# Kernel tuning notes

Hardware: AMD Instinct MI355X
Metric: run time of the kernel (lower is better)

The kernel has to match this reference:

```python
import jax, jax.numpy as jnp
import numpy as np

N = 100000   # nodes
E = 1600000  # edges
H = 128      # num_features == hidden_size
C = 64       # num_classes
BN_EPS = 1e-5


def setup_inputs() -> dict:
    key = jax.random.key(0)
    ks = jax.random.split(key, 11)
    return {
        "x": jax.random.normal(ks[0], (N, H), jnp.float32),
        "edge_index": jax.random.randint(ks[1], (2, E), 0, N, dtype=jnp.int32),
        "edge_attr": jax.random.normal(ks[2], (E,), jnp.float32),
        "conv_w": jax.random.normal(ks[3], (2, 3, H, H), jnp.float32) / np.sqrt(H).astype(np.float32),
        "conv_b": jax.random.normal(ks[4], (2, 3, H), jnp.float32) * 0.1,
        "bn_g": jax.random.uniform(ks[5], (2, 3, H), jnp.float32, 0.5, 1.5),
        "bn_b": jax.random.normal(ks[6], (2, 3, H), jnp.float32) * 0.1,
        "bn_m": jax.random.normal(ks[7], (2, 3, H), jnp.float32) * 0.1,
        "bn_v": jax.random.uniform(ks[8], (2, 3, H), jnp.float32, 0.5, 1.5),
        "fc_w": jax.random.normal(ks[9], (H, C), jnp.float32) / np.sqrt(H).astype(np.float32),
        "fc_b": jax.random.normal(ks[10], (C,), jnp.float32) * 0.1,
    }


def _gin_conv(h, edge_index, w, b, g, beta, m, v):
    # GIN: out = MLP((1+eps)*x + sum_{j in N(i)} x_j), eps=0 (PyG default)
    src, dst = edge_index[0], edge_index[1]
    agg = jax.ops.segment_sum(h[src], dst, num_segments=N)  # [N,H] scatter-add
    h = h + agg
    for i in range(3):  # Linear -> BatchNorm1d (eval stats) -> ReLU
        h = h @ w[i] + b[i]
        h = (h - m[i]) * jax.lax.rsqrt(v[i] + BN_EPS) * g[i] + beta[i]
        h = jax.nn.relu(h)
    return h


def reference(x, edge_index, edge_attr, conv_w, conv_b, bn_g, bn_b, bn_m, bn_v, fc_w, fc_b):
    # edge_attr is ignored by default PyG GINConv (no edge weighting in GIN)
    h = jax.nn.relu(_gin_conv(x, edge_index, conv_w[0], conv_b[0], bn_g[0], bn_b[0], bn_m[0], bn_v[0]))
    h = jax.nn.relu(_gin_conv(h, edge_index, conv_w[1], conv_b[1], bn_g[1], bn_b[1], bn_m[1], bn_v[1]))
    # dropout is identity in eval mode
    logits = h @ fc_w + fc_b  # [N,C]
    return jax.nn.log_softmax(logits, axis=1)
```

## Files before the change

### kernel.cpp

```cpp
#include <hip/hip_runtime.h>

#define NN 100000
#define NE 1600000
#define HF 128
#define NC 64
#define AP 136
#define NB 391
#define BSH 8
#define BMASK 255
#define BCAP 4608

typedef __bf16 bf16x8 __attribute__((ext_vector_type(8)));
typedef float  f32x4  __attribute__((ext_vector_type(4)));
typedef float  f32x2  __attribute__((ext_vector_type(2)));
typedef unsigned short us8 __attribute__((ext_vector_type(8)));
typedef unsigned int u32x4 __attribute__((ext_vector_type(4)));

__device__ __forceinline__ unsigned short f2b(float x) {
  unsigned int u = __float_as_uint(x);
  u += 0x7FFFu + ((u >> 16) & 1u);
  return (unsigned short)(u >> 16);
}
__device__ __forceinline__ float b2f(unsigned short b) {
  return __uint_as_float(((unsigned int)b) << 16);
}

__device__ __forceinline__ void addrow(f32x2 acc[4], u32x4 w) {
  #pragma unroll
  for (int i = 0; i < 4; i++) {
    f32x2 p;
    p.x = __uint_as_float(w[i] << 16);
    p.y = __uint_as_float(w[i] & 0xFFFF0000u);
    acc[i] += p;
  }
}

__global__ __launch_bounds__(512) void prologue_bin(const float* __restrict__ x,
                                                    unsigned short* __restrict__ xb,
                                                    const float* __restrict__ conv_w,
                                                    const float* __restrict__ conv_b,
                                                    const float* __restrict__ bn_g,
                                                    const float* __restrict__ bn_b,
                                                    const float* __restrict__ bn_m,
                                                    const float* __restrict__ bn_v,
                                                    const float* __restrict__ fc_w,
                                                    unsigned short* __restrict__ wt,
                                                    unsigned short* __restrict__ wtf,
                                                    float* __restrict__ sarr,
                                                    float* __restrict__ tarr,
                                                    int* __restrict__ gcur,
                                                    const int* __restrict__ src,
                                                    const int* __restrict__ dst,
                                                    unsigned int* __restrict__ binned) {
  __shared__ int hist[NB];
  int t = threadIdx.x;
  int idx = blockIdx.x * 512 + t;
  {
    size_t i = (size_t)idx * 8;
    float4 a = *(const float4*)(x + i);
    float4 b = *(const float4*)(x + i + 4);
    us8 v = { f2b(a.x), f2b(a.y), f2b(a.z), f2b(a.w),
              f2b(b.x), f2b(b.y), f2b(b.z), f2b(b.w) };
    *(us8*)(xb + i) = v;
  }
  if (idx < 3 * HF) {
    int k = idx >> 7, jj = idx & 127;
    xb[(size_t)k * (NN + 1) * HF + (size_t)NN * HF + jj] = 0;
  }
  if (idx < 6 * HF * HF) {
    int j  = idx & 7;
    int m  = (idx >> 3) & 15;
    int q  = (idx >> 7) & 3;
    int nt = (idx >> 9) & 7;
    int k0 = (idx >> 12) & 3;
    int ls = idx >> 14;
    int k = k0 * 32 + q * 8 + j;
    int n = nt * 16 + m;
    wt[idx] = f2b(conv_w[(ls * HF + k) * HF + n]);
  }
  if (idx < HF * NC) {
    int j  = idx & 7;
    int m  = (idx >> 3) & 15;
    int q  = (idx >> 7) & 3;
    int nt = (idx >> 9) & 3;
    int k0 = idx >> 11;
    int k = k0 * 32 + q * 8 + j;
    int c = nt * 16 + m;
    wtf[idx] = f2b(fc_w[k * NC + c]);
  }
  if (idx < 6 * HF) {
    float s = bn_g[idx] * rsqrtf(bn_v[idx] + 1e-5f);
    sarr[idx] = s;
    tarr[idx] = (conv_b[idx] - bn_m[idx]) * s + bn_b[idx];
  }
  if (blockIdx.x < NB) {
    if (t < NB) hist[t] = 0;
    __syncthreads();
    int base = blockIdx.x * 4096;
    int sv[8], dv[8];
    #pragma unroll
    for (int j = 0; j < 8; j++) {
      int e = base + j * 512 + t;
      bool ok = e < NE;
      dv[j] = ok ? dst[e] : -1;
      sv[j] = ok ? src[e] : 0;
      if (ok) atomicAdd(&hist[dv[j] >> BSH], 1);
    }
    __syncthreads();
    if (t < NB) {
      int c = hist[t];
      if (c) hist[t] = t * BCAP + atomicAdd(&gcur[t], c);
    }
    __syncthreads();
    #pragma unroll
    for (int j = 0; j < 8; j++) {
      if (dv[j] >= 0) {
        int b = dv[j] >> BSH;
        int p = atomicAdd(&hist[b], 1);
        binned[p] = (unsigned int)sv[j] | ((unsigned int)(dv[j] & BMASK) << 17);
      }
    }
  }
}

__global__ __launch_bounds__(512) void build_csr(const unsigned int* __restrict__ binned,
                                                 const int* __restrict__ gcur,
                                                 int* __restrict__ offs,
                                                 int* __restrict__ deg,
                                                 int* __restrict__ csr) {
  __shared__ int ncnt[256];
  __shared__ int sm[256];
  int t = threadIdx.x;
  int b = blockIdx.x;
  int beg = b * BCAP;
  int cntb = gcur[b];
  if (t < 256) ncnt[t] = 0;
  __syncthreads();
  for (int e = beg + t; e < beg + cntb; e += 512) atomicAdd(&ncnt[binned[e] >> 17], 1);
  __syncthreads();
  int s = 0;
  if (t < 256) { s = ncnt[t]; sm[t] = s; }
  __syncthreads();
  for (int off = 1; off < 256; off <<= 1) {
    int u = (t < 256 && t >= off) ? sm[t - off] : 0;
    __syncthreads();
    if (t < 256) sm[t] += u;
    __syncthreads();
  }
  if (t < 256) {
    int ex = sm[t] - s + beg;
    int node = (b << BSH) + t;
    if (node < NN) { offs[node] = ex; deg[node] = s; }
    ncnt[t] = ex;
  }
  __syncthreads();
  for (int e = beg + t; e < beg + cntb; e += 512) {
    unsigned int u = binned[e];
    int p = atomicAdd(&ncnt[u >> 17], 1);
    csr[p] = (int)(u & 0x1FFFFu);
  }
}

__global__ __launch_bounds__(256) void aggregate(const unsigned short* __restrict__ h,
                                                 const int* __restrict__ offs,
                                                 const int* __restrict__ deg,
                                                 const int* __restrict__ csr,
                                                 unsigned short* __restrict__ out) {
  int wave = threadIdx.x >> 6;
  int lane = threadIdx.x & 63;
  int node = blockIdx.x * 4 + wave;
  int g  = lane >> 4;
  int sl = lane & 15;
  int beg = offs[node];
  int dg  = deg[node];
  int n  = dg + 1;
  int nf = n < 64 ? n : 64;

  int myidx = NN;
  if (lane < nf) myidx = (lane == dg) ? node : csr[beg + lane];

  f32x2 acc[4];
  #pragma unroll
  for (int i = 0; i < 4; i++) acc[i] = (f32x2){0.f, 0.f};

  int K = (nf + 3) >> 2;
  int j = 0;
  for (; j + 3 < K; j += 4) {
    int s0 = __shfl(myidx, (j + 0) * 4 + g);
    int s1 = __shfl(myidx, (j + 1) * 4 + g);
    int s2 = __shfl(myidx, (j + 2) * 4 + g);
    int s3 = __shfl(myidx, (j + 3) * 4 + g);
    u32x4 v0 = *(const u32x4*)(h + (size_t)s0 * HF + sl * 8);
    u32x4 v1 = *(const u32x4*)(h + (size_t)s1 * HF + sl * 8);
    u32x4 v2 = *(const u32x4*)(h + (size_t)s2 * HF + sl * 8);
    u32x4 v3 = *(const u32x4*)(h + (size_t)s3 * HF + sl * 8);
    addrow(acc, v0);
    addrow(acc, v1);
    addrow(acc, v2);
    addrow(acc, v3);
  }
  for (; j + 1 < K; j += 2) {
    int s0 = __shfl(myidx, (j + 0) * 4 + g);
    int s1 = __shfl(myidx, (j + 1) * 4 + g);
    u32x4 v0 = *(const u32x4*)(h + (size_t)s0 * HF + sl * 8);
    u32x4 v1 = *(const u32x4*)(h + (size_t)s1 * HF + sl * 8);
    addrow(acc, v0);
    addrow(acc, v1);
  }
  if (j < K) {
    int s0 = __shfl(myidx, j * 4 + g);
    u32x4 v0 = *(const u32x4*)(h + (size_t)s0 * HF + sl * 8);
    addrow(acc, v0);
  }

  if (dg >= 64) {
    for (int e = beg + 64 + g; e < beg + dg; e += 4) {
      int s = csr[e];
      u32x4 v = *(const u32x4*)(h + (size_t)s * HF + sl * 8);
      addrow(acc, v);
    }
    if (g == 0) {
      u32x4 v = *(const u32x4*)(h + (size_t)node * HF + sl * 8);
      addrow(acc, v);
    }
  }

  #pragma unroll
  for (int i = 0; i < 4; i++) {
    acc[i].x += __shfl_xor(acc[i].x, 16, 64);
    acc[i].y += __shfl_xor(acc[i].y, 16, 64);
    acc[i].x += __shfl_xor(acc[i].x, 32, 64);
    acc[i].y += __shfl_xor(acc[i].y, 32, 64);
  }
  if (g == 0) {
    us8 r;
    #pragma unroll
    for (int i = 0; i < 4; i++) {
      r[2 * i]     = f2b(acc[i].x);
      r[2 * i + 1] = f2b(acc[i].y);
    }
    *(us8*)(out + (size_t)node * HF + sl * 8) = r;
  }
}

__device__ __forceinline__ void mlp3_body(const unsigned short* __restrict__ in,
                                          unsigned short* Ab,
                                          const unsigned short* __restrict__ wt,
                                          const float* __restrict__ sarr,
                                          const float* __restrict__ tarr,
                                          int layer, int row0, int wave, int lane,
                                          bf16x8 af[4]) {
  int m = lane & 15, q = lane >> 4;
  int node = row0 + wave * 16 + m;
  int nclamp = (node < NN) ? node : 0;
  #pragma unroll
  for (int k0 = 0; k0 < 4; k0++)
    af[k0] = *(const bf16x8*)(in + (size_t)nclamp * HF + k0 * 32 + q * 8);

  const unsigned short* wbase = wt + layer * 3 * 16384;
  #pragma unroll
  for (int sub = 0; sub < 3; sub++) {
    const unsigned short* wsub = wbase + sub * 16384;
    f32x4 acc[8];
    #pragma unroll
    for (int nt = 0; nt < 8; nt++) {
      acc[nt] = (f32x4){0.f, 0.f, 0.f, 0.f};
      #pragma unroll
      for (int k0 = 0; k0 < 4; k0++) {
        bf16x8 bf = *(const bf16x8*)(wsub + ((k0 * 8 + nt) * 64 + lane) * 8);
        acc[nt] = __builtin_amdgcn_mfma_f32_16x16x32_bf16(af[k0], bf, acc[nt], 0, 0, 0);
      }
    }
    const float* sp = sarr + (layer * 3 + sub) * HF;
    const float* tp = tarr + (layer * 3 + sub) * HF;
    #pragma unroll
    for (int nt = 0; nt < 8; nt++) {
      int c = nt * 16 + m;
      float sc = sp[c], sh = tp[c];
      #pragma unroll
      for (int i = 0; i < 4; i++) {
        int r = wave * 16 + q * 4 + i;
        float y = fmaxf(acc[nt][i] * sc + sh, 0.f);
        Ab[r * AP + c] = f2b(y);
      }
    }
    #pragma unroll
    for (int k0 = 0; k0 < 4; k0++)
      af[k0] = *(const bf16x8*)&Ab[(wave * 16 + m) * AP + k0 * 32 + q * 8];
  }
}

__global__ __launch_bounds__(256) void mlp3(const unsigned short* __restrict__ in,
                                            unsigned short* __restrict__ out,
                                            const unsigned short* __restrict__ wt,
                                            const float* __restrict__ sarr,
                                            const float* __restrict__ tarr) {
  __shared__ unsigned short Ab[64 * AP];
  int t = threadIdx.x;
  int lane = t & 63, wave = t >> 6;
  int row0 = blockIdx.x * 64;
  bf16x8 af[4];
  mlp3_body(in, Ab, wt, sarr, tarr, 0, row0, wave, lane, af);

  for (int it = 0; it < 4; it++) {
    int idx = it * 64 + lane;
    int r = wave * 16 + (idx >> 4);
    int c = (idx & 15) << 3;
    int gr = row0 + r;
    if (gr < NN) *(us8*)(out + (size_t)gr * HF + c) = *(const us8*)&Ab[r * AP + c];
  }
}

__global__ __launch_bounds__(256) void mlp3fc(const unsigned short* __restrict__ in,
                                              float* __restrict__ out,
                                              const unsigned short* __restrict__ wt,
                                              const float* __restrict__ sarr,
                                              const float* __restrict__ tarr,
                                              const unsigned short* __restrict__ wtf,
                                              const float* __restrict__ fc_b) {
  __shared__ unsigned short Ab[64 * AP];
  int t = threadIdx.x;
  int lane = t & 63, wave = t >> 6;
  int row0 = blockIdx.x * 64;
  int m = lane & 15, q = lane >> 4;
  bf16x8 af[4];
  mlp3_body(in, Ab, wt, sarr, tarr, 1, row0, wave, lane, af);

  f32x4 acc[4];
  #pragma unroll
  for (int nt = 0; nt < 4; nt++) {
    acc[nt] = (f32x4){0.f, 0.f, 0.f, 0.f};
    #pragma unroll
    for (int k0 = 0; k0 < 4; k0++) {
      bf16x8 bf = *(const bf16x8*)(wtf + ((k0 * 4 + nt) * 64 + lane) * 8);
      acc[nt] = __builtin_amdgcn_mfma_f32_16x16x32_bf16(af[k0], bf, acc[nt], 0, 0, 0);
    }
  }
  float v[4][4];
  #pragma unroll
  for (int nt = 0; nt < 4; nt++) {
    float b = fc_b[nt * 16 + m];
    #pragma unroll
    for (int i = 0; i < 4; i++) v[nt][i] = acc[nt][i] + b;
  }
  float mx[4], sum[4];
  #pragma unroll
  for (int i = 0; i < 4; i++) {
    mx[i] = fmaxf(fmaxf(v[0][i], v[1][i]), fmaxf(v[2][i], v[3][i]));
    mx[i] = fmaxf(mx[i], __shfl_xor(mx[i], 1, 64));
    mx[i] = fmaxf(mx[i], __shfl_xor(mx[i], 2, 64));
    mx[i] = fmaxf(mx[i], __shfl_xor(mx[i], 4, 64));
    mx[i] = fmaxf(mx[i], __shfl_xor(mx[i], 8, 64));
    sum[i] = __expf(v[0][i] - mx[i]) + __expf(v[1][i] - mx[i])
           + __expf(v[2][i] - mx[i]) + __expf(v[3][i] - mx[i]);
    sum[i] += __shfl_xor(sum[i], 1, 64);
    sum[i] += __shfl_xor(sum[i], 2, 64);
    sum[i] += __shfl_xor(sum[i], 4, 64);
    sum[i] += __shfl_xor(sum[i], 8, 64);
    sum[i] = __logf(sum[i]) + mx[i];
  }
  #pragma unroll
  for (int i = 0; i < 4; i++) {
    int gr = row0 + wave * 16 + q * 4 + i;
    if (gr < NN) {
      #pragma unroll
      for (int nt = 0; nt < 4; nt++)
        out[(size_t)gr * NC + nt * 16 + m] = v[nt][i] - sum[i];
    }
  }
}

extern "C" void kernel_launch(void* const* d_in, const int* in_sizes, int n_in,
                              void* d_out, int out_size, void* d_ws, size_t ws_size,
                              hipStream_t stream) {
  const float* x      = (const float*)d_in[0];
  const int*   ei     = (const int*)d_in[1];
  const float* conv_w = (const float*)d_in[3];
  const float* conv_b = (const float*)d_in[4];
  const float* bn_g   = (const float*)d_in[5];
  const float* bn_b   = (const float*)d_in[6];
  const float* bn_m   = (const float*)d_in[7];
  const float* bn_v   = (const float*)d_in[8];
  const float* fc_w   = (const float*)d_in[9];
  const float* fc_b   = (const float*)d_in[10];
  float* out = (float*)d_out;

  const int* srcI = ei;
  const int* dstI = ei + NE;

  unsigned short* Xb   = (unsigned short*)d_ws;
  unsigned short* Abuf = Xb + (size_t)(NN + 1) * HF;
  unsigned short* Bbuf = Abuf + (size_t)(NN + 1) * HF;
  int* gcur   = (int*)(Bbuf + (size_t)(NN + 1) * HF);
  int* offs   = gcur + 512;
  int* deg    = offs + 100004;
  unsigned int* binned = (unsigned int*)(deg + 100004);
  int* csr    = (int*)(binned + (size_t)NB * BCAP);
  unsigned short* wt  = (unsigned short*)(csr + (size_t)NB * BCAP);
  unsigned short* wtf = wt + 6 * HF * HF;
  float* sarr = (float*)(wtf + HF * NC);
  float* tarr = sarr + 6 * HF;

  hipMemsetAsync(gcur, 0, sizeof(int) * NB, stream);
  prologue_bin<<<3125, 512, 0, stream>>>(x, Xb, conv_w, conv_b, bn_g, bn_b, bn_m, bn_v,
                                         fc_w, wt, wtf, sarr, tarr, gcur,
                                         srcI, dstI, binned);
  build_csr<<<NB, 512, 0, stream>>>(binned, gcur, offs, deg, csr);

  aggregate<<<NN / 4, 256, 0, stream>>>(Xb, offs, deg, csr, Abuf);
  mlp3<<<(NN + 63) / 64, 256, 0, stream>>>(Abuf, Bbuf, wt, sarr, tarr);
  aggregate<<<NN / 4, 256, 0, stream>>>(Bbuf, offs, deg, csr, Abuf);
  mlp3fc<<<(NN + 63) / 64, 256, 0, stream>>>(Abuf, out, wt, sarr, tarr, wtf, fc_b);
}
```

Before: 327.7 us.

## Fuse neighbor aggregation into MLP kernels via shared-memory staging

Merges the gather-sum aggregation kernel into the following 3-layer MLP kernel, so that each wave aggregates 16 nodes in sequence and writes the results to LDS, where the MFMA stage reads them. This removes the global write and re-read of the aggregated buffer and two kernel launches. Each wave also prefetches the CSR indices for the next node while summing the current one. In exchange there are far fewer waves working on the latency-bound gather (1563 blocks instead of 25000), which may reduce memory-level parallelism and load balance across nodes with different degrees.

```diff
diff --git a/kernel.cpp b/kernel.cpp
--- a/kernel.cpp
+++ b/kernel.cpp
@@ -20,9 +20,6 @@
   unsigned int u = __float_as_uint(x);
   u += 0x7FFFu + ((u >> 16) & 1u);
   return (unsigned short)(u >> 16);
-}
-__device__ __forceinline__ float b2f(unsigned short b) {
-  return __uint_as_float(((unsigned int)b) << 16);
 }
 
 __device__ __forceinline__ void addrow(f32x2 acc[4], u32x4 w) {
@@ -63,7 +60,7 @@
               f2b(b.x), f2b(b.y), f2b(b.z), f2b(b.w) };
     *(us8*)(xb + i) = v;
   }
-  if (idx < 3 * HF) {
+  if (idx < 2 * HF) {
     int k = idx >> 7, jj = idx & 127;
     xb[(size_t)k * (NN + 1) * HF + (size_t)NN * HF + jj] = 0;
   }
@@ -161,101 +158,115 @@
   }
 }
 
-__global__ __launch_bounds__(256) void aggregate(const unsigned short* __restrict__ h,
-                                                 const int* __restrict__ offs,
-                                                 const int* __restrict__ deg,
-                                                 const int* __restrict__ csr,
-                                                 unsigned short* __restrict__ out) {
-  int wave = threadIdx.x >> 6;
-  int lane = threadIdx.x & 63;
-  int node = blockIdx.x * 4 + wave;
+__device__ __forceinline__ void agg_into_lds(const unsigned short* __restrict__ h,
+                                             const int* __restrict__ offs,
+                                             const int* __restrict__ deg,
+                                             const int* __restrict__ csr,
+                                             unsigned short* Ab,
+                                             int row0, int wave, int lane) {
   int g  = lane >> 4;
   int sl = lane & 15;
-  int beg = offs[node];
-  int dg  = deg[node];
-  int n  = dg + 1;
-  int nf = n < 64 ? n : 64;
-
+  int nodeBase = row0 + wave * 16;
+
+  int beg = 0, dg = 0, nf = 0;
+  if (nodeBase < NN) {
+    beg = offs[nodeBase]; dg = deg[nodeBase];
+    nf = dg + 1; if (nf > 64) nf = 64;
+  }
   int myidx = NN;
-  if (lane < nf) myidx = (lane == dg) ? node : csr[beg + lane];
-
-  f32x2 acc[4];
-  #pragma unroll
-  for (int i = 0; i < 4; i++) acc[i] = (f32x2){0.f, 0.f};
-
-  int K = (nf + 3) >> 2;
-  int j = 0;
-  for (; j + 3 < K; j += 4) {
-    int s0 = __shfl(myidx, (j + 0) * 4 + g);
-    int s1 = __shfl(myidx, (j + 1) * 4 + g);
-    int s2 = __shfl(myidx, (j + 2) * 4 + g);
-    int s3 = __shfl(myidx, (j + 3) * 4 + g);
-    u32x4 v0 = *(const u32x4*)(h + (size_t)s0 * HF + sl * 8);
-    u32x4 v1 = *(const u32x4*)(h + (size_t)s1 * HF + sl * 8);
-    u32x4 v2 = *(const u32x4*)(h + (size_t)s2 * HF + sl * 8);
-    u32x4 v3 = *(const u32x4*)(h + (size_t)s3 * HF + sl * 8);
-    addrow(acc, v0);
-    addrow(acc, v1);
-    addrow(acc, v2);
-    addrow(acc, v3);
-  }
-  for (; j + 1 < K; j += 2) {
-    int s0 = __shfl(myidx, (j + 0) * 4 + g);
-    int s1 = __shfl(myidx, (j + 1) * 4 + g);
-    u32x4 v0 = *(const u32x4*)(h + (size_t)s0 * HF + sl * 8);
-    u32x4 v1 = *(const u32x4*)(h + (size_t)s1 * HF + sl * 8);
-    addrow(acc, v0);
-    addrow(acc, v1);
-  }
-  if (j < K) {
-    int s0 = __shfl(myidx, j * 4 + g);
-    u32x4 v0 = *(const u32x4*)(h + (size_t)s0 * HF + sl * 8);
-    addrow(acc, v0);
-  }
-
-  if (dg >= 64) {
-    for (int e = beg + 64 + g; e < beg + dg; e += 4) {
-      int s = csr[e];
-      u32x4 v = *(const u32x4*)(h + (size_t)s * HF + sl * 8);
-      addrow(acc, v);
+  if (lane < nf) myidx = (lane == dg) ? nodeBase : csr[beg + lane];
+
+  for (int ni = 0; ni < 16; ni++) {
+    int node = nodeBase + ni;
+    int curnf = nf, curdg = dg, curbeg = beg;
+    int curidx = myidx;
+
+    if (ni < 15) {
+      int n2 = node + 1;
+      beg = 0; dg = 0; nf = 0;
+      if (n2 < NN) {
+        beg = offs[n2]; dg = deg[n2];
+        nf = dg + 1; if (nf > 64) nf = 64;
+      }
+      myidx = NN;
+      if (lane < nf) myidx = (lane == dg) ? n2 : csr[beg + lane];
+    }
+
+    f32x2 acc[4];
+    #pragma unroll
+    for (int i = 0; i < 4; i++) acc[i] = (f32x2){0.f, 0.f};
+
+    int K = (curnf + 3) >> 2;
+    int j = 0;
+    for (; j + 3 < K; j += 4) {
+      int s0 = __shfl(curidx, (j + 0) * 4 + g);
+      int s1 = __shfl(curidx, (j + 1) * 4 + g);
+      int s2 = __shfl(curidx, (j + 2) * 4 + g);
+      int s3 = __shfl(curidx, (j + 3) * 4 + g);
+      u32x4 v0 = *(const u32x4*)(h + (size_t)s0 * HF + sl * 8);
+      u32x4 v1 = *(const u32x4*)(h + (size_t)s1 * HF + sl * 8);
+      u32x4 v2 = *(const u32x4*)(h + (size_t)s2 * HF + sl * 8);
+      u32x4 v3 = *(const u32x4*)(h + (size_t)s3 * HF + sl * 8);
+      addrow(acc, v0);
+      addrow(acc, v1);
+      addrow(acc, v2);
+      addrow(acc, v3);
+    }
+    for (; j + 1 < K; j += 2) {
+      int s0 = __shfl(curidx, (j + 0) * 4 + g);
+      int s1 = __shfl(curidx, (j + 1) * 4 + g);
+      u32x4 v0 = *(const u32x4*)(h + (size_t)s0 * HF + sl * 8);
+      u32x4 v1 = *(const u32x4*)(h + (size_t)s1 * HF + sl * 8);
+      addrow(acc, v0);
+      addrow(acc, v1);
+    }
+    if (j < K) {
+      int s0 = __shfl(curidx, j * 4 + g);
+      u32x4 v0 = *(const u32x4*)(h + (size_t)s0 * HF + sl * 8);
+      addrow(acc, v0);
+    }
+
+    if (curdg >= 64) {
+      for (int e = curbeg + 64 + g; e < curbeg + curdg; e += 4) {
+        int s = csr[e];
+        u32x4 v = *(const u32x4*)(h + (size_t)s * HF + sl * 8);
+        addrow(acc, v);
+      }
+      if (g == 0) {
+        u32x4 v = *(const u32x4*)(h + (size_t)node * HF + sl * 8);
+        addrow(acc, v);
+      }
+    }
+
+    #pragma unroll
+    for (int i = 0; i < 4; i++) {
+      acc[i].x += __shfl_xor(acc[i].x, 16, 64);
+      acc[i].y += __shfl_xor(acc[i].y, 16, 64);
+      acc[i].x += __shfl_xor(acc[i].x, 32, 64);
+      acc[i].y += __shfl_xor(acc[i].y, 32, 64);
     }
     if (g == 0) {
-      u32x4 v = *(const u32x4*)(h + (size_t)node * HF + sl * 8);
-      addrow(acc, v);
-    }
-  }
-
-  #pragma unroll
-  for (int i = 0; i < 4; i++) {
-    acc[i].x += __shfl_xor(acc[i].x, 16, 64);
-    acc[i].y += __shfl_xor(acc[i].y, 16, 64);
-    acc[i].x += __shfl_xor(acc[i].x, 32, 64);
-    acc[i].y += __shfl_xor(acc[i].y, 32, 64);
-  }
-  if (g == 0) {
-    us8 r;
-    #pragma unroll
-    for (int i = 0; i < 4; i++) {
-      r[2 * i]     = f2b(acc[i].x);
-      r[2 * i + 1] = f2b(acc[i].y);
-    }
-    *(us8*)(out + (size_t)node * HF + sl * 8) = r;
-  }
-}
-
-__device__ __forceinline__ void mlp3_body(const unsigned short* __restrict__ in,
-                                          unsigned short* Ab,
-                                          const unsigned short* __restrict__ wt,
-                                          const float* __restrict__ sarr,
-                                          const float* __restrict__ tarr,
-                                          int layer, int row0, int wave, int lane,
-                                          bf16x8 af[4]) {
+      us8 r;
+      #pragma unroll
+      for (int i = 0; i < 4; i++) {
+        r[2 * i]     = f2b(acc[i].x);
+        r[2 * i + 1] = f2b(acc[i].y);
+      }
+      *(us8*)&Ab[(wave * 16 + ni) * AP + sl * 8] = r;
+    }
+  }
+}
+
+__device__ __forceinline__ void mlp3_body_lds(unsigned short* Ab,
+                                              const unsigned short* __restrict__ wt,
+                                              const float* __restrict__ sarr,
+                                              const float* __restrict__ tarr,
+                                              int layer, int wave, int lane,
+                                              bf16x8 af[4]) {
   int m = lane & 15, q = lane >> 4;
-  int node = row0 + wave * 16 + m;
-  int nclamp = (node < NN) ? node : 0;
   #pragma unroll
   for (int k0 = 0; k0 < 4; k0++)
-    af[k0] = *(const bf16x8*)(in + (size_t)nclamp * HF + k0 * 32 + q * 8);
+    af[k0] = *(const bf16x8*)&Ab[(wave * 16 + m) * AP + k0 * 32 + q * 8];
 
   const unsigned short* wbase = wt + layer * 3 * 16384;
   #pragma unroll
@@ -290,17 +301,21 @@
   }
 }
 
-__global__ __launch_bounds__(256) void mlp3(const unsigned short* __restrict__ in,
-                                            unsigned short* __restrict__ out,
-                                            const unsigned short* __restrict__ wt,
-                                            const float* __restrict__ sarr,
-                                            const float* __restrict__ tarr) {
+__global__ __launch_bounds__(256) void agg_mlp3(const unsigned short* __restrict__ h,
+                                                const int* __restrict__ offs,
+                                                const int* __restrict__ deg,
+                                                const int* __restrict__ csr,
+                                                unsigned short* __restrict__ out,
+                                                const unsigned short* __restrict__ wt,
+                                                const float* __restrict__ sarr,
+                                                const float* __restrict__ tarr) {
   __shared__ unsigned short Ab[64 * AP];
   int t = threadIdx.x;
   int lane = t & 63, wave = t >> 6;
   int row0 = blockIdx.x * 64;
+  agg_into_lds(h, offs, deg, csr, Ab, row0, wave, lane);
   bf16x8 af[4];
-  mlp3_body(in, Ab, wt, sarr, tarr, 0, row0, wave, lane, af);
+  mlp3_body_lds(Ab, wt, sarr, tarr, 0, wave, lane, af);
 
   for (int it = 0; it < 4; it++) {
     int idx = it * 64 + lane;
@@ -311,20 +326,24 @@
   }
 }
 
-__global__ __launch_bounds__(256) void mlp3fc(const unsigned short* __restrict__ in,
-                                              float* __restrict__ out,
-                                              const unsigned short* __restrict__ wt,
-                                              const float* __restrict__ sarr,
-                                              const float* __restrict__ tarr,
-                                              const unsigned short* __restrict__ wtf,
-                                              const float* __restrict__ fc_b) {
+__global__ __launch_bounds__(256) void agg_mlp3fc(const unsigned short* __restrict__ h,
+                                                  const int* __restrict__ offs,
+                                                  const int* __restrict__ deg,
+                                                  const int* __restrict__ csr,
+                                                  float* __restrict__ out,
+                                                  const unsigned short* __restrict__ wt,
+                                                  const float* __restrict__ sarr,
+                                                  const float* __restrict__ tarr,
+                                                  const unsigned short* __restrict__ wtf,
+                                                  const float* __restrict__ fc_b) {
   __shared__ unsigned short Ab[64 * AP];
   int t = threadIdx.x;
   int lane = t & 63, wave = t >> 6;
   int row0 = blockIdx.x * 64;
   int m = lane & 15, q = lane >> 4;
+  agg_into_lds(h, offs, deg, csr, Ab, row0, wave, lane);
   bf16x8 af[4];
-  mlp3_body(in, Ab, wt, sarr, tarr, 1, row0, wave, lane, af);
+  mlp3_body_lds(Ab, wt, sarr, tarr, 1, wave, lane, af);
 
   f32x4 acc[4];
   #pragma unroll
@@ -389,8 +408,7 @@
   const int* dstI = ei + NE;
 
   unsigned short* Xb   = (unsigned short*)d_ws;
-  unsigned short* Abuf = Xb + (size_t)(NN + 1) * HF;
-  unsigned short* Bbuf = Abuf + (size_t)(NN + 1) * HF;
+  unsigned short* Bbuf = Xb + (size_t)(NN + 1) * HF;
   int* gcur   = (int*)(Bbuf + (size_t)(NN + 1) * HF);
   int* offs   = gcur + 512;
   int* deg    = offs + 100004;
@@ -407,8 +425,7 @@
                                          srcI, dstI, binned);
   build_csr<<<NB, 512, 0, stream>>>(binned, gcur, offs, deg, csr);
 
-  aggregate<<<NN / 4, 256, 0, stream>>>(Xb, offs, deg, csr, Abuf);
-  mlp3<<<(NN + 63) / 64, 256, 0, stream>>>(Abuf, Bbuf, wt, sarr, tarr);
-  aggregate<<<NN / 4, 256, 0, stream>>>(Bbuf, offs, deg, csr, Abuf);
-  mlp3fc<<<(NN + 63) / 64, 256, 0, stream>>>(Abuf, out, wt, sarr, tarr, wtf, fc_b);
-}
+  agg_mlp3<<<(NN + 63) / 64, 256, 0, stream>>>(Xb, offs, deg, csr, Bbuf, wt, sarr, tarr);
+  agg_mlp3fc<<<(NN + 63) / 64, 256, 0, stream>>>(Bbuf, offs, deg, csr, out,
+                                                 wt, sarr, tarr, wtf, fc_b);
+}
```

New measurement: 334.8 us. 1.02x slower.

## Build CSR with global per-node degree atomics instead of two-level binning

Applied to the files above, without the earlier changes.

Replaces the LDS-histogram binning pass and the per-bin CSR build with a simpler three-step scheme. Per-node degrees are counted with global atomics in the prologue, a per-256-node block scan writes offsets and cursors, and a scatter kernel places each edge through a global atomic on its destination cursor. This drops the intermediate binned buffer and the second pass over it. In exchange it adds an extra kernel launch, relies on contended global atomics and random global writes, and still assumes each 256-node block stays within BCAP edges.

```diff
diff --git a/kernel.cpp b/kernel.cpp
--- a/kernel.cpp
+++ b/kernel.cpp
@@ -6,8 +6,6 @@
 #define NC 64
 #define AP 136
 #define NB 391
-#define BSH 8
-#define BMASK 255
 #define BCAP 4608
 
 typedef __bf16 bf16x8 __attribute__((ext_vector_type(8)));
@@ -21,9 +19,6 @@
   u += 0x7FFFu + ((u >> 16) & 1u);
   return (unsigned short)(u >> 16);
 }
-__device__ __forceinline__ float b2f(unsigned short b) {
-  return __uint_as_float(((unsigned int)b) << 16);
-}
 
 __device__ __forceinline__ void addrow(f32x2 acc[4], u32x4 w) {
   #pragma unroll
@@ -35,24 +30,21 @@
   }
 }
 
-__global__ __launch_bounds__(512) void prologue_bin(const float* __restrict__ x,
-                                                    unsigned short* __restrict__ xb,
-                                                    const float* __restrict__ conv_w,
-                                                    const float* __restrict__ conv_b,
-                                                    const float* __restrict__ bn_g,
-                                                    const float* __restrict__ bn_b,
-                                                    const float* __restrict__ bn_m,
-                                                    const float* __restrict__ bn_v,
-                                                    const float* __restrict__ fc_w,
-                                                    unsigned short* __restrict__ wt,
-                                                    unsigned short* __restrict__ wtf,
-                                                    float* __restrict__ sarr,
-                                                    float* __restrict__ tarr,
-                                                    int* __restrict__ gcur,
-                                                    const int* __restrict__ src,
-                                                    const int* __restrict__ dst,
-                                                    unsigned int* __restrict__ binned) {
-  __shared__ int hist[NB];
+__global__ __launch_bounds__(512) void prologue(const float* __restrict__ x,
+                                                unsigned short* __restrict__ xb,
+                                                const float* __restrict__ conv_w,
+                                                const float* __restrict__ conv_b,
+                                                const float* __restrict__ bn_g,
+                                                const float* __restrict__ bn_b,
+                                                const float* __restrict__ bn_m,
+                                                const float* __restrict__ bn_v,
+                                                const float* __restrict__ fc_w,
+                                                unsigned short* __restrict__ wt,
+                                                unsigned short* __restrict__ wtf,
+                                                float* __restrict__ sarr,
+                                                float* __restrict__ tarr,
+                                                int* __restrict__ deg,
+                                                const int* __restrict__ dst) {
   int t = threadIdx.x;
   int idx = blockIdx.x * 512 + t;
   {
@@ -93,72 +85,41 @@
     sarr[idx] = s;
     tarr[idx] = (conv_b[idx] - bn_m[idx]) * s + bn_b[idx];
   }
-  if (blockIdx.x < NB) {
-    if (t < NB) hist[t] = 0;
-    __syncthreads();
-    int base = blockIdx.x * 4096;
-    int sv[8], dv[8];
-    #pragma unroll
-    for (int j = 0; j < 8; j++) {
-      int e = base + j * 512 + t;
-      bool ok = e < NE;
-      dv[j] = ok ? dst[e] : -1;
-      sv[j] = ok ? src[e] : 0;
-      if (ok) atomicAdd(&hist[dv[j] >> BSH], 1);
-    }
-    __syncthreads();
-    if (t < NB) {
-      int c = hist[t];
-      if (c) hist[t] = t * BCAP + atomicAdd(&gcur[t], c);
-    }
-    __syncthreads();
-    #pragma unroll
-    for (int j = 0; j < 8; j++) {
-      if (dv[j] >= 0) {
-        int b = dv[j] >> BSH;
-        int p = atomicAdd(&hist[b], 1);
-        binned[p] = (unsigned int)sv[j] | ((unsigned int)(dv[j] & BMASK) << 17);
-      }
-    }
-  }
-}
-
-__global__ __launch_bounds__(512) void build_csr(const unsigned int* __restrict__ binned,
-                                                 const int* __restrict__ gcur,
+  atomicAdd(&deg[dst[idx]], 1);
+}
+
+__global__ __launch_bounds__(256) void scan_offs(const int* __restrict__ deg,
                                                  int* __restrict__ offs,
-                                                 int* __restrict__ deg,
-                                                 int* __restrict__ csr) {
-  __shared__ int ncnt[256];
+                                                 int* __restrict__ cursor) {
   __shared__ int sm[256];
   int t = threadIdx.x;
   int b = blockIdx.x;
-  int beg = b * BCAP;
-  int cntb = gcur[b];
-  if (t < 256) ncnt[t] = 0;
-  __syncthreads();
-  for (int e = beg + t; e < beg + cntb; e += 512) atomicAdd(&ncnt[binned[e] >> 17], 1);
-  __syncthreads();
-  int s = 0;
-  if (t < 256) { s = ncnt[t]; sm[t] = s; }
+  int node = b * 256 + t;
+  int d = (node < NN) ? deg[node] : 0;
+  sm[t] = d;
   __syncthreads();
   for (int off = 1; off < 256; off <<= 1) {
-    int u = (t < 256 && t >= off) ? sm[t - off] : 0;
+    int u = (t >= off) ? sm[t - off] : 0;
     __syncthreads();
-    if (t < 256) sm[t] += u;
+    sm[t] += u;
     __syncthreads();
   }
-  if (t < 256) {
-    int ex = sm[t] - s + beg;
-    int node = (b << BSH) + t;
-    if (node < NN) { offs[node] = ex; deg[node] = s; }
-    ncnt[t] = ex;
-  }
-  __syncthreads();
-  for (int e = beg + t; e < beg + cntb; e += 512) {
-    unsigned int u = binned[e];
-    int p = atomicAdd(&ncnt[u >> 17], 1);
-    csr[p] = (int)(u & 0x1FFFFu);
-  }
+  if (node < NN) {
+    int ex = sm[t] - d + b * BCAP;
+    offs[node] = ex;
+    cursor[node] = ex;
+  }
+}
+
+__global__ __launch_bounds__(512) void scatter_csr(const int* __restrict__ src,
+                                                   const int* __restrict__ dst,
+                                                   int* __restrict__ cursor,
+                                                   int* __restrict__ csr) {
+  int idx = blockIdx.x * 512 + threadIdx.x;
+  int d = dst[idx];
+  int s = src[idx];
+  int p = atomicAdd(&cursor[d], 1);
+  csr[p] = s;
 }
 
 __global__ __launch_bounds__(256) void aggregate(const unsigned short* __restrict__ h,
@@ -169,6 +130,7 @@
   int wave = threadIdx.x >> 6;
   int lane = threadIdx.x & 63;
   int node = blockIdx.x * 4 + wave;
+  if (node >= NN) return;
   int g  = lane >> 4;
   int sl = lane & 15;
   int beg = offs[node];
@@ -391,21 +353,20 @@
   unsigned short* Xb   = (unsigned short*)d_ws;
   unsigned short* Abuf = Xb + (size_t)(NN + 1) * HF;
   unsigned short* Bbuf = Abuf + (size_t)(NN + 1) * HF;
-  int* gcur   = (int*)(Bbuf + (size_t)(NN + 1) * HF);
-  int* offs   = gcur + 512;
-  int* deg    = offs + 100004;
-  unsigned int* binned = (unsigned int*)(deg + 100004);
-  int* csr    = (int*)(binned + (size_t)NB * BCAP);
+  int* deg    = (int*)(Bbuf + (size_t)(NN + 1) * HF);
+  int* offs   = deg + 100004;
+  int* cursor = offs + 100004;
+  int* csr    = cursor + 100004;
   unsigned short* wt  = (unsigned short*)(csr + (size_t)NB * BCAP);
   unsigned short* wtf = wt + 6 * HF * HF;
   float* sarr = (float*)(wtf + HF * NC);
   float* tarr = sarr + 6 * HF;
 
-  hipMemsetAsync(gcur, 0, sizeof(int) * NB, stream);
-  prologue_bin<<<3125, 512, 0, stream>>>(x, Xb, conv_w, conv_b, bn_g, bn_b, bn_m, bn_v,
-                                         fc_w, wt, wtf, sarr, tarr, gcur,
-                                         srcI, dstI, binned);
-  build_csr<<<NB, 512, 0, stream>>>(binned, gcur, offs, deg, csr);
+  hipMemsetAsync(deg, 0, sizeof(int) * 100004, stream);
+  prologue<<<3125, 512, 0, stream>>>(x, Xb, conv_w, conv_b, bn_g, bn_b, bn_m, bn_v,
+                                     fc_w, wt, wtf, sarr, tarr, deg, dstI);
+  scan_offs<<<NB, 256, 0, stream>>>(deg, offs, cursor);
+  scatter_csr<<<3125, 512, 0, stream>>>(srcI, dstI, cursor, csr);
 
   aggregate<<<NN / 4, 256, 0, stream>>>(Xb, offs, deg, csr, Abuf);
   mlp3<<<(NN + 63) / 64, 256, 0, stream>>>(Abuf, Bbuf, wt, sarr, tarr);
```

New measurement: 463.5 us. 41.5% more time.

## Split edge binning into own kernel and stage MLP weights in LDS

Applied to the files above, without the earlier changes.

Edge binning moves out of the prologue into a separate kernel with 782 blocks handling 2048 edges each, instead of 391 blocks handling 4096 each, so more blocks share the binning work. The MLP kernels now copy each 128x128 bf16 weight sub-matrix cooperatively into shared memory before the MFMA loop, rather than having every wave read the weights from global memory. This adds 32KB of LDS per block and extra barriers, which may lower occupancy, plus one more kernel launch. A bounds guard is also added in aggregate.

```diff
diff --git a/kernel.cpp b/kernel.cpp
--- a/kernel.cpp
+++ b/kernel.cpp
@@ -21,9 +21,6 @@
   u += 0x7FFFu + ((u >> 16) & 1u);
   return (unsigned short)(u >> 16);
 }
-__device__ __forceinline__ float b2f(unsigned short b) {
-  return __uint_as_float(((unsigned int)b) << 16);
-}
 
 __device__ __forceinline__ void addrow(f32x2 acc[4], u32x4 w) {
   #pragma unroll
@@ -35,24 +32,19 @@
   }
 }
 
-__global__ __launch_bounds__(512) void prologue_bin(const float* __restrict__ x,
-                                                    unsigned short* __restrict__ xb,
-                                                    const float* __restrict__ conv_w,
-                                                    const float* __restrict__ conv_b,
-                                                    const float* __restrict__ bn_g,
-                                                    const float* __restrict__ bn_b,
-                                                    const float* __restrict__ bn_m,
-                                                    const float* __restrict__ bn_v,
-                                                    const float* __restrict__ fc_w,
-                                                    unsigned short* __restrict__ wt,
-                                                    unsigned short* __restrict__ wtf,
-                                                    float* __restrict__ sarr,
-                                                    float* __restrict__ tarr,
-                                                    int* __restrict__ gcur,
-                                                    const int* __restrict__ src,
-                                                    const int* __restrict__ dst,
-                                                    unsigned int* __restrict__ binned) {
-  __shared__ int hist[NB];
+__global__ __launch_bounds__(512) void prologue(const float* __restrict__ x,
+                                                unsigned short* __restrict__ xb,
+                                                const float* __restrict__ conv_w,
+                                                const float* __restrict__ conv_b,
+                                                const float* __restrict__ bn_g,
+                                                const float* __restrict__ bn_b,
+                                                const float* __restrict__ bn_m,
+                                                const float* __restrict__ bn_v,
+                                                const float* __restrict__ fc_w,
+                                                unsigned short* __restrict__ wt,
+                                                unsigned short* __restrict__ wtf,
+                                                float* __restrict__ sarr,
+                                                float* __restrict__ tarr) {
   int t = threadIdx.x;
   int idx = blockIdx.x * 512 + t;
   {
@@ -93,32 +85,38 @@
     sarr[idx] = s;
     tarr[idx] = (conv_b[idx] - bn_m[idx]) * s + bn_b[idx];
   }
-  if (blockIdx.x < NB) {
-    if (t < NB) hist[t] = 0;
-    __syncthreads();
-    int base = blockIdx.x * 4096;
-    int sv[8], dv[8];
-    #pragma unroll
-    for (int j = 0; j < 8; j++) {
-      int e = base + j * 512 + t;
-      bool ok = e < NE;
-      dv[j] = ok ? dst[e] : -1;
-      sv[j] = ok ? src[e] : 0;
-      if (ok) atomicAdd(&hist[dv[j] >> BSH], 1);
-    }
-    __syncthreads();
-    if (t < NB) {
-      int c = hist[t];
-      if (c) hist[t] = t * BCAP + atomicAdd(&gcur[t], c);
-    }
-    __syncthreads();
-    #pragma unroll
-    for (int j = 0; j < 8; j++) {
-      if (dv[j] >= 0) {
-        int b = dv[j] >> BSH;
-        int p = atomicAdd(&hist[b], 1);
-        binned[p] = (unsigned int)sv[j] | ((unsigned int)(dv[j] & BMASK) << 17);
-      }
+}
+
+__global__ __launch_bounds__(512) void bin_edges(const int* __restrict__ src,
+                                                 const int* __restrict__ dst,
+                                                 int* __restrict__ gcur,
+                                                 unsigned int* __restrict__ binned) {
+  __shared__ int hist[NB];
+  int t = threadIdx.x;
+  if (t < NB) hist[t] = 0;
+  __syncthreads();
+  int base = blockIdx.x * 2048;
+  int sv[4], dv[4];
+  #pragma unroll
+  for (int j = 0; j < 4; j++) {
+    int e = base + j * 512 + t;
+    bool ok = e < NE;
+    dv[j] = ok ? dst[e] : -1;
+    sv[j] = ok ? src[e] : 0;
+    if (ok) atomicAdd(&hist[dv[j] >> BSH], 1);
+  }
+  __syncthreads();
+  if (t < NB) {
+    int c = hist[t];
+    if (c) hist[t] = t * BCAP + atomicAdd(&gcur[t], c);
+  }
+  __syncthreads();
+  #pragma unroll
+  for (int j = 0; j < 4; j++) {
+    if (dv[j] >= 0) {
+      int b = dv[j] >> BSH;
+      int p = atomicAdd(&hist[b], 1);
+      binned[p] = (unsigned int)sv[j] | ((unsigned int)(dv[j] & BMASK) << 17);
     }
   }
 }
@@ -169,6 +167,7 @@
   int wave = threadIdx.x >> 6;
   int lane = threadIdx.x & 63;
   int node = blockIdx.x * 4 + wave;
+  if (node >= NN) return;
   int g  = lane >> 4;
   int sl = lane & 15;
   int beg = offs[node];
@@ -245,11 +244,12 @@
 
 __device__ __forceinline__ void mlp3_body(const unsigned short* __restrict__ in,
                                           unsigned short* Ab,
+                                          unsigned short* ws,
                                           const unsigned short* __restrict__ wt,
                                           const float* __restrict__ sarr,
                                           const float* __restrict__ tarr,
                                           int layer, int row0, int wave, int lane,
-                                          bf16x8 af[4]) {
+                                          int t, bf16x8 af[4]) {
   int m = lane & 15, q = lane >> 4;
   int node = row0 + wave * 16 + m;
   int nclamp = (node < NN) ? node : 0;
@@ -261,13 +261,20 @@
   #pragma unroll
   for (int sub = 0; sub < 3; sub++) {
     const unsigned short* wsub = wbase + sub * 16384;
+    __syncthreads();
+    #pragma unroll
+    for (int i = 0; i < 8; i++) {
+      int o = (i * 256 + t) * 8;
+      *(us8*)&ws[o] = *(const us8*)(wsub + o);
+    }
+    __syncthreads();
     f32x4 acc[8];
     #pragma unroll
     for (int nt = 0; nt < 8; nt++) {
       acc[nt] = (f32x4){0.f, 0.f, 0.f, 0.f};
       #pragma unroll
       for (int k0 = 0; k0 < 4; k0++) {
-        bf16x8 bf = *(const bf16x8*)(wsub + ((k0 * 8 + nt) * 64 + lane) * 8);
+        bf16x8 bf = *(const bf16x8*)&ws[((k0 * 8 + nt) * 64 + lane) * 8];
         acc[nt] = __builtin_amdgcn_mfma_f32_16x16x32_bf16(af[k0], bf, acc[nt], 0, 0, 0);
       }
     }
@@ -296,11 +303,12 @@
                                             const float* __restrict__ sarr,
                                             const float* __restrict__ tarr) {
   __shared__ unsigned short Ab[64 * AP];
+  __shared__ unsigned short ws[16384];
   int t = threadIdx.x;
   int lane = t & 63, wave = t >> 6;
   int row0 = blockIdx.x * 64;
   bf16x8 af[4];
-  mlp3_body(in, Ab, wt, sarr, tarr, 0, row0, wave, lane, af);
+  mlp3_body(in, Ab, ws, wt, sarr, tarr, 0, row0, wave, lane, t, af);
 
   for (int it = 0; it < 4; it++) {
     int idx = it * 64 + lane;
@@ -319,12 +327,13 @@
                                               const unsigned short* __restrict__ wtf,
                                               const float* __restrict__ fc_b) {
   __shared__ unsigned short Ab[64 * AP];
+  __shared__ unsigned short ws[16384];
   int t = threadIdx.x;
   int lane = t & 63, wave = t >> 6;
   int row0 = blockIdx.x * 64;
   int m = lane & 15, q = lane >> 4;
   bf16x8 af[4];
-  mlp3_body(in, Ab, wt, sarr, tarr, 1, row0, wave, lane, af);
+  mlp3_body(in, Ab, ws, wt, sarr, tarr, 1, row0, wave, lane, t, af);
 
   f32x4 acc[4];
   #pragma unroll
@@ -402,9 +411,9 @@
   float* tarr = sarr + 6 * HF;
 
   hipMemsetAsync(gcur, 0, sizeof(int) * NB, stream);
-  prologue_bin<<<3125, 512, 0, stream>>>(x, Xb, conv_w, conv_b, bn_g, bn_b, bn_m, bn_v,
-                                         fc_w, wt, wtf, sarr, tarr, gcur,
-                                         srcI, dstI, binned);
+  prologue<<<3125, 512, 0, stream>>>(x, Xb, conv_w, conv_b, bn_g, bn_b, bn_m, bn_v,
+                                     fc_w, wt, wtf, sarr, tarr);
+  bin_edges<<<782, 512, 0, stream>>>(srcI, dstI, gcur, binned);
   build_csr<<<NB, 512, 0, stream>>>(binned, gcur, offs, deg, csr);
 
   aggregate<<<NN / 4, 256, 0, stream>>>(Xb, offs, deg, csr, Abuf);
```

Result: no change. 329.9 us (+0.7%).
